# Performance work log

Hardware: AMD Instinct MI355X
Metric: run time of the kernel (lower is better)

The kernel has to match this reference:

```python
import jax, jax.numpy as jnp
import numpy as np

OFFSET = 3  # windows 3,5,7


def _maxpool_same(x, k):
    # MaxPool2d(kernel=k, stride=1, padding=(k-1)//2); torch pads with -inf
    p = (k - 1) // 2
    return jax.lax.reduce_window(
        x, -jnp.inf, jax.lax.max,
        window_dimensions=(1, 1, k, k),
        window_strides=(1, 1, 1, 1),
        padding=((0, 0), (0, 0), (p, p), (p, p)))


def setup_inputs() -> dict:
    key = jax.random.key(0)
    # strictly positive so log10 is finite
    x = jax.random.uniform(key, (8, 64, 256, 256), dtype=jnp.float32,
                           minval=1e-3, maxval=1.0)
    return {"x": x}


def reference(x) -> jnp.ndarray:
    B, C, H, W = x.shape
    windows = jnp.array([2.0 * i + 1.0 for i in range(1, OFFSET + 1)],
                        dtype=x.dtype)  # [3,5,7]
    xs = jnp.log10(windows / (H * W))
    xc = xs - xs.mean()
    # Closed-form OLS slope weights: inv(X X^T) X reduces analytically to
    # w_i = (x_i - xbar) / sum_j (x_j - xbar)^2 for the slope row.
    w = xc / jnp.sum(xc * xc)                  # [OFFSET]
    # slope = sum_i w_i * log10(maxpool_{k_i}(x)), computed without stacking
    holder = jnp.zeros_like(x)
    for i in range(OFFSET):
        k = 2 * (i + 1) + 1
        holder = holder + w[i] * jnp.log10(_maxpool_same(x, k))
    return holder  # (B, C, H, W)
```

## Files before the change

kernel.cpp:

```cpp
#include <hip/hip_runtime.h>
#include <cmath>


#define IMG_H 256
#define IMG_W 256
#define RPW   16
#define CH    4

typedef float vf4 __attribute__((ext_vector_type(4)));

__device__ __forceinline__ vf4 aload(const float* base, uint32_t voff) {
  vf4 r;
  asm volatile("global_load_dwordx4 %0, %1, %2"
               : "=v"(r) : "v"(voff), "s"(base) : "memory");
  return r;
}

__device__ __forceinline__ void wait4(vf4& a, vf4& b, vf4& c, vf4& d) {
  asm volatile("s_waitcnt vmcnt(4)"
               : "+v"(a), "+v"(b), "+v"(c), "+v"(d) :: "memory");
}

__device__ __forceinline__ void wait0_10(vf4& a, vf4& b, vf4& c, vf4& d,
                                         vf4& e, vf4& f, vf4& g, vf4& h,
                                         vf4& i, vf4& j) {
  asm volatile("s_waitcnt vmcnt(0)"
               : "+v"(a), "+v"(b), "+v"(c), "+v"(d), "+v"(e),
                 "+v"(f), "+v"(g), "+v"(h), "+v"(i), "+v"(j) :: "memory");
}

__device__ __forceinline__ float dpp_left(float v) {
  return __int_as_float(
      __builtin_amdgcn_update_dpp(0, __float_as_int(v), 0x138, 0xF, 0xF, true));
}
__device__ __forceinline__ float dpp_right(float v) {
  return __int_as_float(
      __builtin_amdgcn_update_dpp(0, __float_as_int(v), 0x130, 0xF, 0xF, true));
}

__device__ __forceinline__ vf4 vmax(vf4 a, vf4 b) {
  vf4 r;
  r.x = fmaxf(a.x, b.x); r.y = fmaxf(a.y, b.y);
  r.z = fmaxf(a.z, b.z); r.w = fmaxf(a.w, b.w);
  return r;
}

struct PS { float p1, p2, p3, s1, s2, s3, f; };

__device__ __forceinline__ PS make_ps(vf4 a) {
  PS r;
  r.p1 = a.x;
  r.p2 = fmaxf(a.x, a.y);
  r.p3 = fmaxf(r.p2, a.z);
  r.s1 = a.w;
  r.s2 = fmaxf(a.z, a.w);
  r.s3 = fmaxf(a.y, r.s2);
  r.f  = fmaxf(r.p2, r.s2);
  return r;
}

__global__ __launch_bounds__(256, 4) void holder_kernel(
    const float* __restrict__ x, float* __restrict__ out,
    float w3, float w5, float w7)
{
  const int lane = threadIdx.x & 63;
  const int wave = threadIdx.x >> 6;
  const int img  = blockIdx.x;
  const int band = blockIdx.y;
  const int r0   = band * (4 * RPW) + wave * RPW;

  const float* px = x + (size_t)img * (IMG_H * IMG_W);
  float*       po = out + (size_t)img * (IMG_H * IMG_W) + lane * 4;
  const uint32_t lo = (uint32_t)lane * 16u;

  const vf4 vzero = (vf4)0.0f;

  vf4 w[10];
#pragma unroll
  for (int i = 0; i < 10; ++i) {
    int rr = r0 - 3 + i;
    int rc = rr < 0 ? 0 : (rr > IMG_H - 1 ? IMG_H - 1 : rr);
    w[i] = aload(px, (uint32_t)(rc * IMG_W * 4) + lo);
  }
  wait0_10(w[0], w[1], w[2], w[3], w[4], w[5], w[6], w[7], w[8], w[9]);
#pragma unroll
  for (int i = 0; i < 10; ++i) {
    int rr = r0 - 3 + i;
    if (rr < 0 || rr >= IMG_H) w[i] = vzero;
  }

#pragma unroll
  for (int c = 0; c < RPW / CH; ++c) {
    const int R = r0 + c * CH;

    vf4 nw[CH];
#pragma unroll
    for (int j = 0; j < CH; ++j) {
      int rr = R + 7 + j;
      int rc = rr > IMG_H - 1 ? IMG_H - 1 : rr;
      nw[j] = aload(px, (uint32_t)(rc * IMG_W * 4) + lo);
    }

#pragma unroll
    for (int j = 0; j < CH; ++j) {
      vf4 v1 = vmax(vmax(w[j + 2], w[j + 3]), w[j + 4]);
      vf4 v2 = vmax(v1, vmax(w[j + 1], w[j + 5]));
      vf4 v3 = vmax(v2, vmax(w[j + 0], w[j + 6]));

      PS a1 = make_ps(v1), a2 = make_ps(v2), a3 = make_ps(v3);

      float L1s1 = dpp_left(a1.s1);
      float L2s1 = dpp_left(a2.s1);
      float L2s2 = dpp_left(a2.s2);
      float L3s1 = dpp_left(a3.s1);
      float L3s2 = dpp_left(a3.s2);
      float L3s3 = dpp_left(a3.s3);

      float R1p1 = dpp_right(a1.p1);
      float R2p1 = dpp_right(a2.p1);
      float R2p2 = dpp_right(a2.p2);
      float R3p1 = dpp_right(a3.p1);
      float R3p2 = dpp_right(a3.p2);
      float R3p3 = dpp_right(a3.p3);

      float m3_0 = fmaxf(L1s1, a1.p2);
      float m3_1 = a1.p3;
      float m3_2 = a1.s3;
      float m3_3 = fmaxf(a1.s2, R1p1);

      float m5_0 = fmaxf(L2s2, a2.p3);
      float m5_1 = fmaxf(L2s1, a2.f);
      float m5_2 = fmaxf(a2.f, R2p1);
      float m5_3 = fmaxf(a2.s3, R2p2);

      float m7_0 = fmaxf(L3s3, a3.f);
      float m7_1 = fmaxf(fmaxf(L3s2, a3.f), R3p1);
      float m7_2 = fmaxf(fmaxf(L3s1, a3.f), R3p2);
      float m7_3 = fmaxf(a3.f, R3p3);

      vf4 o;
      o.x = fmaf(w7, __log2f(m7_0), fmaf(w5, __log2f(m5_0), w3 * __log2f(m3_0)));
      o.y = fmaf(w7, __log2f(m7_1), fmaf(w5, __log2f(m5_1), w3 * __log2f(m3_1)));
      o.z = fmaf(w7, __log2f(m7_2), fmaf(w5, __log2f(m5_2), w3 * __log2f(m3_2)));
      o.w = fmaf(w7, __log2f(m7_3), fmaf(w5, __log2f(m5_3), w3 * __log2f(m3_3)));
      __builtin_nontemporal_store(o, (vf4*)(po + (R + j) * IMG_W));
    }

    wait4(nw[0], nw[1], nw[2], nw[3]);

#pragma unroll
    for (int j = 0; j < CH; ++j) {
      int rr = R + 7 + j;
      if (rr >= IMG_H) nw[j] = vzero;
    }
#pragma unroll
    for (int i = 0; i < 10 - CH; ++i) w[i] = w[i + CH];
#pragma unroll
    for (int j = 0; j < CH; ++j) w[10 - CH + j] = nw[j];
  }
}

extern "C" void kernel_launch(void* const* d_in, const int* in_sizes, int n_in,
                              void* d_out, int out_size, void* d_ws, size_t ws_size,
                              hipStream_t stream) {
  const float* x = (const float*)d_in[0];
  float* out = (float*)d_out;

  const int n_img = in_sizes[0] / (IMG_H * IMG_W);

  const double l0 = log10(3.0), l1 = log10(5.0), l2 = log10(7.0);
  const double m  = (l0 + l1 + l2) / 3.0;
  const double c0 = l0 - m, c1 = l1 - m, c2 = l2 - m;
  const double s  = c0 * c0 + c1 * c1 + c2 * c2;
  const double LG2 = 0.30102999566398119521;
  const float w3 = (float)(c0 / s * LG2);
  const float w5 = (float)(c1 / s * LG2);
  const float w7 = (float)(c2 / s * LG2);

  hipLaunchKernelGGL(holder_kernel, dim3(n_img, 4), dim3(256), 0, stream,
                     x, out, w3, w5, w7);
}
```

Baseline: 234.0 us.

## Use single-wave blocks over 8-row bands with all row loads issued upfront

Each block is now a single wave covering an 8-row band, so the grid has many more, smaller blocks. Each wave issues all 14 needed row loads at once. It waits for the first 10 rows to compute the first four output rows, then waits for the last 4 to finish the band. This replaces the chunked streaming loop and is meant to raise memory-level parallelism and hide load latency. The cost is that each wave re-reads more halo rows per output row (14 per 8 instead of 22 per 16), and there are more block launches.

```diff
diff --git a/kernel.cpp b/kernel.cpp
--- a/kernel.cpp
+++ b/kernel.cpp
@@ -4,8 +4,8 @@
 
 #define IMG_H 256
 #define IMG_W 256
-#define RPW   16
-#define CH    4
+#define RPW   8
+#define NR    14
 
 typedef float vf4 __attribute__((ext_vector_type(4)));
 
@@ -16,17 +16,17 @@
   return r;
 }
 
-__device__ __forceinline__ void wait4(vf4& a, vf4& b, vf4& c, vf4& d) {
+__device__ __forceinline__ void wait_first10(vf4& a, vf4& b, vf4& c, vf4& d,
+                                             vf4& e, vf4& f, vf4& g, vf4& h,
+                                             vf4& i, vf4& j) {
+  asm volatile("s_waitcnt vmcnt(4)"
+               : "+v"(a), "+v"(b), "+v"(c), "+v"(d), "+v"(e),
+                 "+v"(f), "+v"(g), "+v"(h), "+v"(i), "+v"(j) :: "memory");
+}
+
+__device__ __forceinline__ void wait_last4(vf4& a, vf4& b, vf4& c, vf4& d) {
   asm volatile("s_waitcnt vmcnt(4)"
                : "+v"(a), "+v"(b), "+v"(c), "+v"(d) :: "memory");
-}
-
-__device__ __forceinline__ void wait0_10(vf4& a, vf4& b, vf4& c, vf4& d,
-                                         vf4& e, vf4& f, vf4& g, vf4& h,
-                                         vf4& i, vf4& j) {
-  asm volatile("s_waitcnt vmcnt(0)"
-               : "+v"(a), "+v"(b), "+v"(c), "+v"(d), "+v"(e),
-                 "+v"(f), "+v"(g), "+v"(h), "+v"(i), "+v"(j) :: "memory");
 }
 
 __device__ __forceinline__ float dpp_left(float v) {
@@ -59,15 +59,60 @@
   return r;
 }
 
-__global__ __launch_bounds__(256, 4) void holder_kernel(
+__device__ __forceinline__ vf4 row_out(vf4 wm3, vf4 wm2, vf4 wm1, vf4 wc,
+                                       vf4 wp1, vf4 wp2, vf4 wp3,
+                                       float w3, float w5, float w7) {
+  vf4 v1 = vmax(vmax(wm1, wc), wp1);
+  vf4 v2 = vmax(v1, vmax(wm2, wp2));
+  vf4 v3 = vmax(v2, vmax(wm3, wp3));
+
+  PS a1 = make_ps(v1), a2 = make_ps(v2), a3 = make_ps(v3);
+
+  float L1s1 = dpp_left(a1.s1);
+  float L2s1 = dpp_left(a2.s1);
+  float L2s2 = dpp_left(a2.s2);
+  float L3s1 = dpp_left(a3.s1);
+  float L3s2 = dpp_left(a3.s2);
+  float L3s3 = dpp_left(a3.s3);
+
+  float R1p1 = dpp_right(a1.p1);
+  float R2p1 = dpp_right(a2.p1);
+  float R2p2 = dpp_right(a2.p2);
+  float R3p1 = dpp_right(a3.p1);
+  float R3p2 = dpp_right(a3.p2);
+  float R3p3 = dpp_right(a3.p3);
+
+  float m3_0 = fmaxf(L1s1, a1.p2);
+  float m3_1 = a1.p3;
+  float m3_2 = a1.s3;
+  float m3_3 = fmaxf(a1.s2, R1p1);
+
+  float m5_0 = fmaxf(L2s2, a2.p3);
+  float m5_1 = fmaxf(L2s1, a2.f);
+  float m5_2 = fmaxf(a2.f, R2p1);
+  float m5_3 = fmaxf(a2.s3, R2p2);
+
+  float m7_0 = fmaxf(L3s3, a3.f);
+  float m7_1 = fmaxf(fmaxf(L3s2, a3.f), R3p1);
+  float m7_2 = fmaxf(fmaxf(L3s1, a3.f), R3p2);
+  float m7_3 = fmaxf(a3.f, R3p3);
+
+  vf4 o;
+  o.x = fmaf(w7, __log2f(m7_0), fmaf(w5, __log2f(m5_0), w3 * __log2f(m3_0)));
+  o.y = fmaf(w7, __log2f(m7_1), fmaf(w5, __log2f(m5_1), w3 * __log2f(m3_1)));
+  o.z = fmaf(w7, __log2f(m7_2), fmaf(w5, __log2f(m5_2), w3 * __log2f(m3_2)));
+  o.w = fmaf(w7, __log2f(m7_3), fmaf(w5, __log2f(m5_3), w3 * __log2f(m3_3)));
+  return o;
+}
+
+__global__ __launch_bounds__(64, 4) void holder_kernel(
     const float* __restrict__ x, float* __restrict__ out,
     float w3, float w5, float w7)
 {
-  const int lane = threadIdx.x & 63;
-  const int wave = threadIdx.x >> 6;
-  const int img  = blockIdx.x;
-  const int band = blockIdx.y;
-  const int r0   = band * (4 * RPW) + wave * RPW;
+  const int lane = threadIdx.x;
+  const int band = blockIdx.x;
+  const int img  = blockIdx.y;
+  const int r0   = band * RPW;
 
   const float* px = x + (size_t)img * (IMG_H * IMG_W);
   float*       po = out + (size_t)img * (IMG_H * IMG_W) + lane * 4;
@@ -75,88 +120,38 @@
 
   const vf4 vzero = (vf4)0.0f;
 
-  vf4 w[10];
+  vf4 w[NR];
 #pragma unroll
-  for (int i = 0; i < 10; ++i) {
+  for (int i = 0; i < NR; ++i) {
     int rr = r0 - 3 + i;
     int rc = rr < 0 ? 0 : (rr > IMG_H - 1 ? IMG_H - 1 : rr);
     w[i] = aload(px, (uint32_t)(rc * IMG_W * 4) + lo);
   }
-  wait0_10(w[0], w[1], w[2], w[3], w[4], w[5], w[6], w[7], w[8], w[9]);
+
+  wait_first10(w[0], w[1], w[2], w[3], w[4], w[5], w[6], w[7], w[8], w[9]);
 #pragma unroll
   for (int i = 0; i < 10; ++i) {
-    int rr = r0 - 3 + i;
-    if (rr < 0 || rr >= IMG_H) w[i] = vzero;
+    if (r0 - 3 + i < 0) w[i] = vzero;
   }
 
 #pragma unroll
-  for (int c = 0; c < RPW / CH; ++c) {
-    const int R = r0 + c * CH;
+  for (int j = 0; j < 4; ++j) {
+    vf4 o = row_out(w[j], w[j + 1], w[j + 2], w[j + 3],
+                    w[j + 4], w[j + 5], w[j + 6], w3, w5, w7);
+    __builtin_nontemporal_store(o, (vf4*)(po + (r0 + j) * IMG_W));
+  }
 
-    vf4 nw[CH];
+  wait_last4(w[10], w[11], w[12], w[13]);
 #pragma unroll
-    for (int j = 0; j < CH; ++j) {
-      int rr = R + 7 + j;
-      int rc = rr > IMG_H - 1 ? IMG_H - 1 : rr;
-      nw[j] = aload(px, (uint32_t)(rc * IMG_W * 4) + lo);
-    }
+  for (int i = 10; i < NR; ++i) {
+    if (r0 - 3 + i >= IMG_H) w[i] = vzero;
+  }
 
 #pragma unroll
-    for (int j = 0; j < CH; ++j) {
-      vf4 v1 = vmax(vmax(w[j + 2], w[j + 3]), w[j + 4]);
-      vf4 v2 = vmax(v1, vmax(w[j + 1], w[j + 5]));
-      vf4 v3 = vmax(v2, vmax(w[j + 0], w[j + 6]));
-
-      PS a1 = make_ps(v1), a2 = make_ps(v2), a3 = make_ps(v3);
-
-      float L1s1 = dpp_left(a1.s1);
-      float L2s1 = dpp_left(a2.s1);
-      float L2s2 = dpp_left(a2.s2);
-      float L3s1 = dpp_left(a3.s1);
-      float L3s2 = dpp_left(a3.s2);
-      float L3s3 = dpp_left(a3.s3);
-
-      float R1p1 = dpp_right(a1.p1);
-      float R2p1 = dpp_right(a2.p1);
-      float R2p2 = dpp_right(a2.p2);
-      float R3p1 = dpp_right(a3.p1);
-      float R3p2 = dpp_right(a3.p2);
-      float R3p3 = dpp_right(a3.p3);
-
-      float m3_0 = fmaxf(L1s1, a1.p2);
-      float m3_1 = a1.p3;
-      float m3_2 = a1.s3;
-      float m3_3 = fmaxf(a1.s2, R1p1);
-
-      float m5_0 = fmaxf(L2s2, a2.p3);
-      float m5_1 = fmaxf(L2s1, a2.f);
-      float m5_2 = fmaxf(a2.f, R2p1);
-      float m5_3 = fmaxf(a2.s3, R2p2);
-
-      float m7_0 = fmaxf(L3s3, a3.f);
-      float m7_1 = fmaxf(fmaxf(L3s2, a3.f), R3p1);
-      float m7_2 = fmaxf(fmaxf(L3s1, a3.f), R3p2);
-      float m7_3 = fmaxf(a3.f, R3p3);
-
-      vf4 o;
-      o.x = fmaf(w7, __log2f(m7_0), fmaf(w5, __log2f(m5_0), w3 * __log2f(m3_0)));
-      o.y = fmaf(w7, __log2f(m7_1), fmaf(w5, __log2f(m5_1), w3 * __log2f(m3_1)));
-      o.z = fmaf(w7, __log2f(m7_2), fmaf(w5, __log2f(m5_2), w3 * __log2f(m3_2)));
-      o.w = fmaf(w7, __log2f(m7_3), fmaf(w5, __log2f(m5_3), w3 * __log2f(m3_3)));
-      __builtin_nontemporal_store(o, (vf4*)(po + (R + j) * IMG_W));
-    }
-
-    wait4(nw[0], nw[1], nw[2], nw[3]);
-
-#pragma unroll
-    for (int j = 0; j < CH; ++j) {
-      int rr = R + 7 + j;
-      if (rr >= IMG_H) nw[j] = vzero;
-    }
-#pragma unroll
-    for (int i = 0; i < 10 - CH; ++i) w[i] = w[i + CH];
-#pragma unroll
-    for (int j = 0; j < CH; ++j) w[10 - CH + j] = nw[j];
+  for (int j = 4; j < 8; ++j) {
+    vf4 o = row_out(w[j], w[j + 1], w[j + 2], w[j + 3],
+                    w[j + 4], w[j + 5], w[j + 6], w3, w5, w7);
+    __builtin_nontemporal_store(o, (vf4*)(po + (r0 + j) * IMG_W));
   }
 }
 
@@ -177,6 +172,6 @@
   const float w5 = (float)(c1 / s * LG2);
   const float w7 = (float)(c2 / s * LG2);
 
-  hipLaunchKernelGGL(holder_kernel, dim3(n_img, 4), dim3(256), 0, stream,
-                     x, out, w3, w5, w7);
+  hipLaunchKernelGGL(holder_kernel, dim3(IMG_H / RPW, n_img), dim3(64), 0,
+                     stream, x, out, w3, w5, w7);
 }
```

Result: no change. 230.5 us (-1.5%).
